# Kernel tuning notes

Hardware: AMD Instinct MI355X
Metric: run time of the kernel (lower is better)

Reference implementation:

```python
import jax, jax.numpy as jnp
import numpy as np

N_NODES = 50000
N_EDGES = 800000
F_IN = 512
HID = 256
N_CLS = 40
W_DIM = 50  # dimension*dimension*2 with dimension=5


def _prelu(x, a):
    return jnp.where(x >= 0, x, a * x)


def _segment_softmax(w, idx, n):
    # per-segment (grouped by idx), per-channel numerically stable softmax
    m = jax.ops.segment_max(w, idx, num_segments=n)
    e = jnp.exp(w - m[idx])
    s = jax.ops.segment_sum(e, idx, num_segments=n)
    return e / s[idx]


def _curvgn(x, edge_index, w_mul, W, b, w0, a, w1, b1):
    n = x.shape[0]
    h = x @ W + b                                   # [N, C]
    ow = _prelu(w_mul @ w0, a) @ w1 + b1            # [E, C] edge-weight MLP
    ow = _segment_softmax(ow, edge_index[0], n)     # softmax grouped by source (as in source)
    msg = ow * h[edge_index[0]]                     # gather x_j, weight
    return jax.ops.segment_sum(msg, edge_index[1], num_segments=n)  # scatter-add at target


def setup_inputs() -> dict:
    key = jax.random.key(0)
    ks = jax.random.split(key, 12)
    s = 0.05
    return {
        "x": jax.random.normal(ks[0], (N_NODES, F_IN), jnp.float32),
        "edge_index": jax.random.randint(ks[1], (2, N_EDGES), 0, N_NODES, jnp.int64 if jax.config.jax_enable_x64 else jnp.int32).astype(jnp.int32),
        "w_mul": jax.random.normal(ks[2], (N_EDGES, W_DIM), jnp.float32),
        "W1": jax.random.normal(ks[3], (F_IN, HID), jnp.float32) * s,
        "b1": jnp.zeros((HID,), jnp.float32),
        "m1_w0": jax.random.normal(ks[4], (W_DIM, HID), jnp.float32) * s,
        "m1_a": jnp.full((HID,), 0.2, jnp.float32),
        "m1_w1": jax.random.normal(ks[5], (HID, HID), jnp.float32) * s,
        "m1_b1": jnp.zeros((HID,), jnp.float32),
        "W2": jax.random.normal(ks[6], (HID, N_CLS), jnp.float32) * s,
        "b2": jnp.zeros((N_CLS,), jnp.float32),
        "m2_w0": jax.random.normal(ks[7], (W_DIM, N_CLS), jnp.float32) * s,
        "m2_a": jnp.full((N_CLS,), 0.2, jnp.float32),
        "m2_w1": jax.random.normal(ks[8], (N_CLS, N_CLS), jnp.float32) * s,
        "m2_b1": jnp.zeros((N_CLS,), jnp.float32),
    }


def reference(x, edge_index, w_mul, W1, b1, m1_w0, m1_a, m1_w1, m1_b1,
              W2, b2, m2_w0, m2_a, m2_w1, m2_b1):
    # eval mode: dropout is identity
    h = _curvgn(x, edge_index, w_mul, W1, b1, m1_w0, m1_a, m1_w1, m1_b1)
    h = jax.nn.elu(h)
    out = _curvgn(h, edge_index, w_mul, W2, b2, m2_w0, m2_a, m2_w1, m2_b1)
    return jax.nn.log_softmax(out, axis=1)
```

## Files before the change

kernel.cpp:

```cpp
#include <hip/hip_runtime.h>
#include <hip/hip_bf16.h>
#include <math.h>

#define N_NODESC 50000
#define N_EDGESC 800000
#define F_INC 512
#define HIDC 256
#define N_CLSC 40
#define W_DIMC 50
#define HN (2*N_NODESC)
#define NB_SCAN 196

typedef __bf16 bf16;
typedef __bf16 bf16x8 __attribute__((ext_vector_type(8)));
typedef __bf16 bf16x4 __attribute__((ext_vector_type(4)));
typedef float  f32x4  __attribute__((ext_vector_type(4)));

__global__ void k_hist(const int* __restrict__ ei, int* __restrict__ hist) {
    int e = blockIdx.x*256 + threadIdx.x;
    if (e < N_EDGESC) {
        atomicAdd(&hist[ei[e]], 1);
        atomicAdd(&hist[N_NODESC + ei[N_EDGESC + e]], 1);
    }
}
__global__ void k_copy(int* d, const int* s, int n) {
    int i = blockIdx.x*256 + threadIdx.x;
    if (i < n) d[i] = s[i];
}
__global__ void k_scan_part(const int* __restrict__ hist, int* __restrict__ part) {
    __shared__ int lds[512];
    int t = threadIdx.x;
    int i = blockIdx.x*512 + t;
    lds[t] = (i < HN) ? hist[i] : 0;
    __syncthreads();
    for (int off = 256; off > 0; off >>= 1) {
        if (t < off) lds[t] += lds[t+off];
        __syncthreads();
    }
    if (t == 0) part[blockIdx.x] = lds[0];
}
__global__ void k_scan_mid(const int* __restrict__ part, int* __restrict__ partx) {
    __shared__ int lds[256];
    int t = threadIdx.x;
    int v = (t < NB_SCAN) ? part[t] : 0;
    lds[t] = v;
    __syncthreads();
    for (int off = 1; off < 256; off <<= 1) {
        int add = (t >= off) ? lds[t-off] : 0;
        __syncthreads();
        lds[t] += add;
        __syncthreads();
    }
    partx[t] = lds[t] - v;
}
__global__ void k_scan_apply(const int* __restrict__ hist, const int* __restrict__ partx,
                             int* __restrict__ basev) {
    __shared__ int lds[512];
    int t = threadIdx.x;
    int i = blockIdx.x*512 + t;
    int v = (i < HN) ? hist[i] : 0;
    lds[t] = v;
    __syncthreads();
    for (int off = 1; off < 512; off <<= 1) {
        int add = (t >= off) ? lds[t-off] : 0;
        __syncthreads();
        lds[t] += add;
        __syncthreads();
    }
    if (i < HN) basev[i] = lds[t] - v + partx[blockIdx.x];
}
__global__ void k_scatter(const int* __restrict__ ei, int* __restrict__ cursor,
                          int* __restrict__ perm_src,
                          int* __restrict__ spd, int* __restrict__ svd) {
    int e = blockIdx.x*256 + threadIdx.x;
    if (e >= N_EDGESC) return;
    int s = ei[e];
    int d = ei[N_EDGESC + e];
    int p = atomicAdd(&cursor[s], 1);
    perm_src[p] = e;
    int q = atomicAdd(&cursor[N_NODESC + d], 1) - N_EDGESC;
    spd[q] = p;
    svd[q] = s;
}

__global__ void k_tconv(const float* __restrict__ src, bf16* __restrict__ dst,
                        int Ks, int Ns, int Kp, int Np) {
    int idx = blockIdx.x*256 + threadIdx.x;
    if (idx >= Kp*Np) return;
    int n = idx / Kp, k = idx - n*Kp;
    float v = (k < Ks && n < Ns) ? src[k*Ns + n] : 0.f;
    dst[idx] = (bf16)v;
}

__global__ __launch_bounds__(256) void k_h1(const float* __restrict__ x,
                                            const bf16* __restrict__ W1t,
                                            const float* __restrict__ b1,
                                            bf16* __restrict__ h1) {
    __shared__ __align__(16) bf16 a_lds[64*40];
    int tid = threadIdx.x;
    int lane = tid & 63, wv = tid >> 6;
    int l15 = lane & 15, quad = lane >> 4;
    int r0 = blockIdx.x * 64;
    f32x4 acc[4][4] = {};
    for (int ks = 0; ks < 16; ++ks) {
        #pragma unroll
        for (int i = 0; i < 2; ++i) {
            int idx = tid + i*256;
            int rl = idx >> 3, c4 = idx & 7;
            int rg = r0 + rl;
            f32x4 v = {};
            if (rg < N_NODESC) v = *(const f32x4*)&x[(size_t)rg*F_INC + ks*32 + c4*4];
            bf16x4 b; b[0]=(bf16)v[0]; b[1]=(bf16)v[1]; b[2]=(bf16)v[2]; b[3]=(bf16)v[3];
            *(bf16x4*)&a_lds[rl*40 + c4*4] = b;
        }
        __syncthreads();
        bf16x8 af[4], bfr[4];
        #pragma unroll
        for (int mt = 0; mt < 4; ++mt)
            af[mt] = *(const bf16x8*)&a_lds[(mt*16 + l15)*40 + quad*8];
        #pragma unroll
        for (int nt = 0; nt < 4; ++nt) {
            int n = wv*64 + nt*16 + l15;
            bfr[nt] = *(const bf16x8*)&W1t[n*F_INC + ks*32 + quad*8];
        }
        #pragma unroll
        for (int mt = 0; mt < 4; ++mt)
            #pragma unroll
            for (int nt = 0; nt < 4; ++nt)
                acc[mt][nt] = __builtin_amdgcn_mfma_f32_16x16x32_bf16(af[mt], bfr[nt], acc[mt][nt], 0, 0, 0);
        __syncthreads();
    }
    #pragma unroll
    for (int nt = 0; nt < 4; ++nt) {
        int col = wv*64 + nt*16 + l15;
        float bias = b1[col];
        #pragma unroll
        for (int mt = 0; mt < 4; ++mt)
            #pragma unroll
            for (int r = 0; r < 4; ++r) {
                int row = r0 + mt*16 + quad*4 + r;
                if (row < N_NODESC) h1[(size_t)row*HIDC + col] = (bf16)(acc[mt][nt][r] + bias);
            }
    }
}

__global__ __launch_bounds__(256) void k_edge(
    const float* __restrict__ w_mul, const int* __restrict__ perm_src,
    const int* __restrict__ ei,
    const bf16* __restrict__ w0t,  const float* __restrict__ a1,
    const bf16* __restrict__ w1t,  const float* __restrict__ bb1,
    const bf16* __restrict__ w20t, const float* __restrict__ a2,
    const bf16* __restrict__ w21t, const float* __restrict__ bb2,
    float* __restrict__ s1, float* __restrict__ s2,
    bf16* __restrict__ eow1, bf16* __restrict__ eow2) {
    __shared__ __align__(16) bf16 wm[64*72];
    __shared__ __align__(16) bf16 t1[64*264];
    __shared__ __align__(16) bf16 t2[64*72];
    __shared__ int e_lds[64], sv[64];
    int tid = threadIdx.x;
    int lane = tid & 63, wv = tid >> 6;
    int l15 = lane & 15, quad = lane >> 4;
    int p0 = blockIdx.x * 64;

    if (tid < 64) {
        int e = perm_src[p0 + tid];
        e_lds[tid] = e;
        sv[tid] = ei[e];
    }
    __syncthreads();
    #pragma unroll
    for (int i = 0; i < 16; ++i) {
        int idx = tid + i*256;
        int r = idx >> 6, k = idx & 63;
        float v = (k < W_DIMC) ? w_mul[(size_t)e_lds[r]*W_DIMC + k] : 0.f;
        wm[r*72 + k] = (bf16)v;
    }
    #pragma unroll
    for (int i = 0; i < 4; ++i) {
        int idx = tid + i*256;
        int r = idx >> 4, c = 48 + (idx & 15);
        t2[r*72 + c] = (bf16)0.f;
    }
    __syncthreads();

    {
        f32x4 acc[4][4] = {};
        #pragma unroll
        for (int ks = 0; ks < 2; ++ks) {
            bf16x8 af[4], bfr[4];
            #pragma unroll
            for (int mt = 0; mt < 4; ++mt)
                af[mt] = *(const bf16x8*)&wm[(mt*16 + l15)*72 + ks*32 + quad*8];
            #pragma unroll
            for (int i = 0; i < 4; ++i) {
                int n = wv*64 + i*16 + l15;
                bfr[i] = *(const bf16x8*)&w0t[n*64 + ks*32 + quad*8];
            }
            #pragma unroll
            for (int mt = 0; mt < 4; ++mt)
                #pragma unroll
                for (int i = 0; i < 4; ++i)
                    acc[mt][i] = __builtin_amdgcn_mfma_f32_16x16x32_bf16(af[mt], bfr[i], acc[mt][i], 0, 0, 0);
        }
        #pragma unroll
        for (int i = 0; i < 4; ++i) {
            int col = wv*64 + i*16 + l15;
            float al = a1[col];
            #pragma unroll
            for (int mt = 0; mt < 4; ++mt)
                #pragma unroll
                for (int r = 0; r < 4; ++r) {
                    float v = acc[mt][i][r];
                    v = (v >= 0.f) ? v : al*v;
                    t1[(mt*16 + quad*4 + r)*264 + col] = (bf16)v;
                }
        }
    }
    __syncthreads();

    {
        f32x4 acc[4][4] = {};
        #pragma unroll
        for (int ks = 0; ks < 8; ++ks) {
            bf16x8 af[4], bfr[4];
            #pragma unroll
            for (int mt = 0; mt < 4; ++mt)
                af[mt] = *(const bf16x8*)&t1[(mt*16 + l15)*264 + ks*32 + quad*8];
            #pragma unroll
            for (int i = 0; i < 4; ++i) {
                int n = wv*64 + i*16 + l15;
                bfr[i] = *(const bf16x8*)&w1t[n*HIDC + ks*32 + quad*8];
            }
            #pragma unroll
            for (int mt = 0; mt < 4; ++mt)
                #pragma unroll
                for (int i = 0; i < 4; ++i)
                    acc[mt][i] = __builtin_amdgcn_mfma_f32_16x16x32_bf16(af[mt], bfr[i], acc[mt][i], 0, 0, 0);
        }
        __syncthreads();
        #pragma unroll
        for (int i = 0; i < 4; ++i) {
            int col = wv*64 + i*16 + l15;
            float bias = bb1[col];
            #pragma unroll
            for (int mt = 0; mt < 4; ++mt)
                #pragma unroll
                for (int r = 0; r < 4; ++r)
                    t1[(mt*16 + quad*4 + r)*264 + col] = (bf16)__expf(acc[mt][i][r] + bias);
        }
    }
    __syncthreads();

    #pragma unroll
    for (int i = 0; i < 8; ++i) {
        int idx = i*256 + tid;
        int row = idx >> 5, c8 = idx & 31;
        bf16x8 v = *(const bf16x8*)&t1[row*264 + c8*8];
        *(bf16x8*)&eow1[(size_t)(p0 + row)*HIDC + c8*8] = v;
    }
    {
        int c = tid;
        float acc = 0.f;
        #pragma unroll 8
        for (int r = 0; r < 64; ++r) {
            acc += (float)t1[r*264 + c];
            if (r == 63 || sv[r+1] != sv[r]) {
                atomicAdd(&s1[(size_t)sv[r]*HIDC + c], acc);
                acc = 0.f;
            }
        }
    }

    {
        f32x4 acc[3] = {};
        #pragma unroll
        for (int ks = 0; ks < 2; ++ks) {
            bf16x8 af = *(const bf16x8*)&wm[(wv*16 + l15)*72 + ks*32 + quad*8];
            #pragma unroll
            for (int i = 0; i < 3; ++i) {
                bf16x8 bfr = *(const bf16x8*)&w20t[(i*16 + l15)*64 + ks*32 + quad*8];
                acc[i] = __builtin_amdgcn_mfma_f32_16x16x32_bf16(af, bfr, acc[i], 0, 0, 0);
            }
        }
        #pragma unroll
        for (int i = 0; i < 3; ++i) {
            int col = i*16 + l15;
            float al = (col < N_CLSC) ? a2[col] : 0.f;
            #pragma unroll
            for (int r = 0; r < 4; ++r) {
                float v = acc[i][r];
                v = (v >= 0.f) ? v : al*v;
                t2[(wv*16 + quad*4 + r)*72 + col] = (bf16)v;
            }
        }
    }
    __syncthreads();

    {
        f32x4 acc[3] = {};
        #pragma unroll
        for (int ks = 0; ks < 2; ++ks) {
            bf16x8 af = *(const bf16x8*)&t2[(wv*16 + l15)*72 + ks*32 + quad*8];
            #pragma unroll
            for (int i = 0; i < 3; ++i) {
                bf16x8 bfr = *(const bf16x8*)&w21t[(i*16 + l15)*64 + ks*32 + quad*8];
                acc[i] = __builtin_amdgcn_mfma_f32_16x16x32_bf16(af, bfr, acc[i], 0, 0, 0);
            }
        }
        __syncthreads();
        #pragma unroll
        for (int i = 0; i < 3; ++i) {
            int col = i*16 + l15;
            if (col < N_CLSC) {
                float bias = bb2[col];
                #pragma unroll
                for (int r = 0; r < 4; ++r)
                    t2[(wv*16 + quad*4 + r)*72 + col] = (bf16)__expf(acc[i][r] + bias);
            }
        }
    }
    __syncthreads();

    #pragma unroll
    for (int i = 0; i < 2; ++i) {
        int idx = i*256 + tid;
        if (idx < 320) {
            int row = idx / 5, c8 = idx % 5;
            bf16x8 v = *(const bf16x8*)&t2[row*72 + c8*8];
            *(bf16x8*)&eow2[(size_t)(p0 + row)*N_CLSC + c8*8] = v;
        }
    }
    if (tid < 240) {
        int c = tid % 40, g = tid / 40;
        int rA = g*11, rB = (rA + 11 < 64) ? rA + 11 : 64;
        float acc = 0.f;
        for (int r = rA; r < rB; ++r) {
            acc += (float)t2[r*72 + c];
            if (r == rB-1 || sv[r+1] != sv[r]) {
                atomicAdd(&s2[(size_t)sv[r]*N_CLSC + c], acc);
                acc = 0.f;
            }
        }
    }
}

__global__ __launch_bounds__(256) void k_agg1(
    const bf16* __restrict__ eow1, const bf16* __restrict__ g1,
    const int* __restrict__ basev, const int* __restrict__ spd,
    const int* __restrict__ svd, float* __restrict__ out1) {
    int v = blockIdx.x, c = threadIdx.x;
    int b = basev[N_NODESC + v] - N_EDGESC;
    int e = (v < N_NODESC-1) ? basev[N_NODESC + v + 1] - N_EDGESC : N_EDGESC;
    float acc = 0.f;
    #pragma unroll 2
    for (int j = b; j < e; ++j) {
        int sp = spd[j], s = svd[j];
        acc += (float)eow1[(size_t)sp*HIDC + c] * (float)g1[(size_t)s*HIDC + c];
    }
    out1[(size_t)v*HIDC + c] = (acc > 0.f) ? acc : expm1f(acc);
}

__global__ __launch_bounds__(64) void k_agg2(
    const bf16* __restrict__ eow2, const bf16* __restrict__ g2,
    const int* __restrict__ basev, const int* __restrict__ spd,
    const int* __restrict__ svd, float* __restrict__ out) {
    int v = blockIdx.x, c = threadIdx.x;
    int b = basev[N_NODESC + v] - N_EDGESC;
    int e = (v < N_NODESC-1) ? basev[N_NODESC + v + 1] - N_EDGESC : N_EDGESC;
    bool act = (c < N_CLSC);
    float acc = 0.f;
    #pragma unroll 2
    for (int j = b; j < e; ++j) {
        int sp = spd[j], s = svd[j];
        if (act) acc += (float)eow2[(size_t)sp*N_CLSC + c] * (float)g2[(size_t)s*N_CLSC + c];
    }
    float m = act ? acc : -INFINITY;
    #pragma unroll
    for (int off = 32; off > 0; off >>= 1) m = fmaxf(m, __shfl_xor(m, off));
    float ex = act ? __expf(acc - m) : 0.f;
    #pragma unroll
    for (int off = 32; off > 0; off >>= 1) ex += __shfl_xor(ex, off);
    if (act) out[(size_t)v*N_CLSC + c] = acc - m - logf(ex);
}

__global__ void k_div_bf4(bf16* __restrict__ h, const float* __restrict__ s, int n4) {
    int i = blockIdx.x*256 + threadIdx.x;
    if (i < n4) {
        bf16x4 hv = *(bf16x4*)&h[i*4];
        f32x4 sv = *(const f32x4*)&s[i*4];
        #pragma unroll
        for (int k = 0; k < 4; ++k) hv[k] = (bf16)((float)hv[k] / sv[k]);
        *(bf16x4*)&h[i*4] = hv;
    }
}
__global__ void k_h2(const float* __restrict__ out1, const float* __restrict__ W2,
                     const float* __restrict__ b2, bf16* __restrict__ h2) {
    int i = blockIdx.x*256 + threadIdx.x;
    if (i >= N_NODESC*N_CLSC) return;
    int v = i / N_CLSC, c = i - v*N_CLSC;
    float acc = b2[c];
    const float* row = &out1[(size_t)v*HIDC];
    #pragma unroll 4
    for (int k = 0; k < HIDC; ++k) acc += row[k] * W2[k*N_CLSC + c];
    h2[i] = (bf16)acc;
}

extern "C" void kernel_launch(void* const* d_in, const int* in_sizes, int n_in,
                              void* d_out, int out_size, void* d_ws, size_t ws_size,
                              hipStream_t stream) {
    const float* x    = (const float*)d_in[0];
    const int*   ei   = (const int*)d_in[1];
    const float* wmul = (const float*)d_in[2];
    const float* W1   = (const float*)d_in[3];
    const float* b1   = (const float*)d_in[4];
    const float* m1w0 = (const float*)d_in[5];
    const float* m1a  = (const float*)d_in[6];
    const float* m1w1 = (const float*)d_in[7];
    const float* m1b1 = (const float*)d_in[8];
    const float* W2   = (const float*)d_in[9];
    const float* b2   = (const float*)d_in[10];
    const float* m2w0 = (const float*)d_in[11];
    const float* m2a  = (const float*)d_in[12];
    const float* m2w1 = (const float*)d_in[13];
    const float* m2b1 = (const float*)d_in[14];
    float* out = (float*)d_out;

    char* ws = (char*)d_ws;
    size_t off = 0;
    auto alloc = [&](size_t bytes) -> void* {
        off = (off + 255) & ~(size_t)255;
        void* p = ws + off;
        off += bytes;
        return p;
    };
    bf16*  h1g1  = (bf16*) alloc((size_t)N_NODESC*HIDC*2);
    float* s1o1  = (float*)alloc((size_t)N_NODESC*HIDC*4);
    bf16*  h2g2  = (bf16*) alloc((size_t)N_NODESC*N_CLSC*2);
    float* s2    = (float*)alloc((size_t)N_NODESC*N_CLSC*4);
    bf16*  W1t   = (bf16*) alloc(256*512*2);
    bf16*  w0t   = (bf16*) alloc(256*64*2);
    bf16*  w1tm  = (bf16*) alloc(256*256*2);
    bf16*  w20t  = (bf16*) alloc(48*64*2);
    bf16*  w21t  = (bf16*) alloc(48*64*2);
    int*   hist  = (int*)  alloc(HN*4);
    int*   basev = (int*)  alloc(HN*4);
    int*   cursor= (int*)  alloc(HN*4);
    int*   part  = (int*)  alloc(256*4);
    int*   partx = (int*)  alloc(256*4);
    int*   perm_src = (int*)alloc((size_t)N_EDGESC*4);
    int*   spd      = (int*)alloc((size_t)N_EDGESC*4);
    int*   svd      = (int*)alloc((size_t)N_EDGESC*4);
    bf16*  eow1  = (bf16*) alloc((size_t)N_EDGESC*HIDC*2);
    bf16*  eow2  = (bf16*) alloc((size_t)N_EDGESC*N_CLSC*2);

    hipMemsetAsync(hist, 0, HN*4, stream);
    hipMemsetAsync(s1o1, 0, (size_t)N_NODESC*HIDC*4, stream);
    hipMemsetAsync(s2,   0, (size_t)N_NODESC*N_CLSC*4, stream);
    k_hist<<<(N_EDGESC+255)/256, 256, 0, stream>>>(ei, hist);
    k_scan_part<<<NB_SCAN, 512, 0, stream>>>(hist, part);
    k_scan_mid<<<1, 256, 0, stream>>>(part, partx);
    k_scan_apply<<<NB_SCAN, 512, 0, stream>>>(hist, partx, basev);
    k_copy<<<(HN+255)/256, 256, 0, stream>>>(cursor, basev, HN);
    k_scatter<<<(N_EDGESC+255)/256, 256, 0, stream>>>(ei, cursor, perm_src, spd, svd);

    k_tconv<<<(512*256+255)/256, 256, 0, stream>>>(W1,   W1t, 512, 256, 512, 256);
    k_tconv<<<(256*64+255)/256,  256, 0, stream>>>(m1w0, w0t,  50, 256,  64, 256);
    k_tconv<<<(256*256+255)/256, 256, 0, stream>>>(m1w1, w1tm, 256, 256, 256, 256);
    k_tconv<<<(48*64+255)/256,   256, 0, stream>>>(m2w0, w20t,  50,  40,  64,  48);
    k_tconv<<<(48*64+255)/256,   256, 0, stream>>>(m2w1, w21t,  40,  40,  64,  48);

    k_h1<<<(N_NODESC+63)/64, 256, 0, stream>>>(x, W1t, b1, h1g1);
    k_edge<<<N_EDGESC/64, 256, 0, stream>>>(wmul, perm_src, ei,
                                            w0t, m1a, w1tm, m1b1,
                                            w20t, m2a, w21t, m2b1,
                                            s1o1, s2, eow1, eow2);
    k_div_bf4<<<(N_NODESC*HIDC/4+255)/256, 256, 0, stream>>>(h1g1, s1o1, N_NODESC*HIDC/4);
    k_agg1<<<N_NODESC, 256, 0, stream>>>(eow1, h1g1, basev, spd, svd, s1o1);

    k_h2<<<(N_NODESC*N_CLSC+255)/256, 256, 0, stream>>>(s1o1, W2, b2, h2g2);
    k_div_bf4<<<(N_NODESC*N_CLSC/4+255)/256, 256, 0, stream>>>(h2g2, s2, N_NODESC*N_CLSC/4);
    k_agg2<<<N_NODESC, 64, 0, stream>>>(eow2, h2g2, basev, spd, svd, out);
}
```

Before: 1.583 ms.

## Split fused edge MLP kernel into three smaller kernels via global intermediate

Breaks the monolithic edge kernel into k_mlp1a (first layer plus PReLU, written to eow1 as a bf16 intermediate), k_mlp1b (second layer, exp, and segment-sum atomics), and k_mlp2 (the class-dimension MLP). Each kernel uses less LDS and fewer registers, which should raise occupancy and latency hiding. The w_mul gather is also vectorized to float2 loads, and w0t is staged in LDS. The cost is an extra round trip of an E x 256 bf16 tensor through global memory, w_mul being read twice, and two more launches.

```diff
diff --git a/kernel.cpp b/kernel.cpp
--- a/kernel.cpp
+++ b/kernel.cpp
@@ -14,7 +14,9 @@
 typedef __bf16 bf16;
 typedef __bf16 bf16x8 __attribute__((ext_vector_type(8)));
 typedef __bf16 bf16x4 __attribute__((ext_vector_type(4)));
+typedef __bf16 bf16x2 __attribute__((ext_vector_type(2)));
 typedef float  f32x4  __attribute__((ext_vector_type(4)));
+typedef float  f32x2  __attribute__((ext_vector_type(2)));
 
 __global__ void k_hist(const int* __restrict__ ei, int* __restrict__ hist) {
     int e = blockIdx.x*256 + threadIdx.x;
@@ -144,17 +146,155 @@
     }
 }
 
-__global__ __launch_bounds__(256) void k_edge(
+__global__ __launch_bounds__(256) void k_mlp1a(
+    const float* __restrict__ w_mul, const int* __restrict__ perm_src,
+    const bf16* __restrict__ w0t, const float* __restrict__ a1,
+    bf16* __restrict__ u1) {
+    __shared__ __align__(16) bf16 wm[64*72];
+    __shared__ __align__(16) bf16 bw[256*72];
+    __shared__ int e_lds[64];
+    int tid = threadIdx.x;
+    int lane = tid & 63, wv = tid >> 6;
+    int l15 = lane & 15, quad = lane >> 4;
+    int p0 = blockIdx.x * 64;
+
+    if (tid < 64) e_lds[tid] = perm_src[p0 + tid];
+    #pragma unroll
+    for (int i = 0; i < 8; ++i) {
+        int idx = i*256 + tid;
+        int n = idx >> 3, j = idx & 7;
+        *(bf16x8*)&bw[n*72 + j*8] = *(const bf16x8*)&w0t[n*64 + j*8];
+    }
+    __syncthreads();
+    #pragma unroll
+    for (int i = 0; i < 7; ++i) {
+        int idx = i*256 + tid;
+        if (idx < 1600) {
+            int row = idx / 25;
+            int k = 2*(idx - row*25);
+            f32x2 v = *(const f32x2*)&w_mul[(size_t)e_lds[row]*W_DIMC + k];
+            bf16x2 b; b[0] = (bf16)v[0]; b[1] = (bf16)v[1];
+            *(bf16x2*)&wm[row*72 + k] = b;
+        }
+    }
+    #pragma unroll
+    for (int i = 0; i < 2; ++i) {
+        int idx = i*256 + tid;
+        if (idx < 448) {
+            int row = idx / 7, c = 50 + 2*(idx - row*7);
+            bf16x2 z; z[0] = (bf16)0.f; z[1] = (bf16)0.f;
+            *(bf16x2*)&wm[row*72 + c] = z;
+        }
+    }
+    __syncthreads();
+
+    f32x4 acc[4][4] = {};
+    #pragma unroll
+    for (int ks = 0; ks < 2; ++ks) {
+        bf16x8 af[4], bfr[4];
+        #pragma unroll
+        for (int mt = 0; mt < 4; ++mt)
+            af[mt] = *(const bf16x8*)&wm[(mt*16 + l15)*72 + ks*32 + quad*8];
+        #pragma unroll
+        for (int i = 0; i < 4; ++i)
+            bfr[i] = *(const bf16x8*)&bw[(wv*64 + i*16 + l15)*72 + ks*32 + quad*8];
+        #pragma unroll
+        for (int mt = 0; mt < 4; ++mt)
+            #pragma unroll
+            for (int i = 0; i < 4; ++i)
+                acc[mt][i] = __builtin_amdgcn_mfma_f32_16x16x32_bf16(af[mt], bfr[i], acc[mt][i], 0, 0, 0);
+    }
+    #pragma unroll
+    for (int i = 0; i < 4; ++i) {
+        int col = wv*64 + i*16 + l15;
+        float al = a1[col];
+        #pragma unroll
+        for (int mt = 0; mt < 4; ++mt)
+            #pragma unroll
+            for (int r = 0; r < 4; ++r) {
+                float v = acc[mt][i][r];
+                v = (v >= 0.f) ? v : al*v;
+                u1[(size_t)(p0 + mt*16 + quad*4 + r)*HIDC + col] = (bf16)v;
+            }
+    }
+}
+
+__global__ __launch_bounds__(256) void k_mlp1b(
+    const int* __restrict__ perm_src, const int* __restrict__ ei,
+    const bf16* __restrict__ w1t, const float* __restrict__ bb1,
+    bf16* __restrict__ eow1,
+    float* __restrict__ s1) {
+    __shared__ __align__(16) bf16 t1[64*264];
+    __shared__ int sv[64];
+    int tid = threadIdx.x;
+    int lane = tid & 63, wv = tid >> 6;
+    int l15 = lane & 15, quad = lane >> 4;
+    int p0 = blockIdx.x * 64;
+
+    if (tid < 64) sv[tid] = ei[perm_src[p0 + tid]];
+    #pragma unroll
+    for (int i = 0; i < 8; ++i) {
+        int idx = i*256 + tid;
+        int row = idx >> 5, j = idx & 31;
+        *(bf16x8*)&t1[row*264 + j*8] = *(const bf16x8*)&eow1[(size_t)(p0 + row)*HIDC + j*8];
+    }
+    __syncthreads();
+
+    f32x4 acc[4][4] = {};
+    #pragma unroll
+    for (int ks = 0; ks < 8; ++ks) {
+        bf16x8 af[4], bfr[4];
+        #pragma unroll
+        for (int mt = 0; mt < 4; ++mt)
+            af[mt] = *(const bf16x8*)&t1[(mt*16 + l15)*264 + ks*32 + quad*8];
+        #pragma unroll
+        for (int i = 0; i < 4; ++i)
+            bfr[i] = *(const bf16x8*)&w1t[(wv*64 + i*16 + l15)*HIDC + ks*32 + quad*8];
+        #pragma unroll
+        for (int mt = 0; mt < 4; ++mt)
+            #pragma unroll
+            for (int i = 0; i < 4; ++i)
+                acc[mt][i] = __builtin_amdgcn_mfma_f32_16x16x32_bf16(af[mt], bfr[i], acc[mt][i], 0, 0, 0);
+    }
+    __syncthreads();
+    #pragma unroll
+    for (int i = 0; i < 4; ++i) {
+        int col = wv*64 + i*16 + l15;
+        float bias = bb1[col];
+        #pragma unroll
+        for (int mt = 0; mt < 4; ++mt)
+            #pragma unroll
+            for (int r = 0; r < 4; ++r)
+                t1[(mt*16 + quad*4 + r)*264 + col] = (bf16)__expf(acc[mt][i][r] + bias);
+    }
+    __syncthreads();
+    #pragma unroll
+    for (int i = 0; i < 8; ++i) {
+        int idx = i*256 + tid;
+        int row = idx >> 5, j = idx & 31;
+        *(bf16x8*)&eow1[(size_t)(p0 + row)*HIDC + j*8] = *(const bf16x8*)&t1[row*264 + j*8];
+    }
+    {
+        int c = tid;
+        float acc2 = 0.f;
+        #pragma unroll
+        for (int r = 0; r < 64; ++r) {
+            acc2 += (float)t1[r*264 + c];
+            if (r == 63 || sv[r+1] != sv[r]) {
+                atomicAdd(&s1[(size_t)sv[r]*HIDC + c], acc2);
+                acc2 = 0.f;
+            }
+        }
+    }
+}
+
+__global__ __launch_bounds__(256) void k_mlp2(
     const float* __restrict__ w_mul, const int* __restrict__ perm_src,
     const int* __restrict__ ei,
-    const bf16* __restrict__ w0t,  const float* __restrict__ a1,
-    const bf16* __restrict__ w1t,  const float* __restrict__ bb1,
     const bf16* __restrict__ w20t, const float* __restrict__ a2,
     const bf16* __restrict__ w21t, const float* __restrict__ bb2,
-    float* __restrict__ s1, float* __restrict__ s2,
-    bf16* __restrict__ eow1, bf16* __restrict__ eow2) {
+    bf16* __restrict__ eow2, float* __restrict__ s2) {
     __shared__ __align__(16) bf16 wm[64*72];
-    __shared__ __align__(16) bf16 t1[64*264];
     __shared__ __align__(16) bf16 t2[64*72];
     __shared__ int e_lds[64], sv[64];
     int tid = threadIdx.x;
@@ -169,107 +309,33 @@
     }
     __syncthreads();
     #pragma unroll
-    for (int i = 0; i < 16; ++i) {
-        int idx = tid + i*256;
-        int r = idx >> 6, k = idx & 63;
-        float v = (k < W_DIMC) ? w_mul[(size_t)e_lds[r]*W_DIMC + k] : 0.f;
-        wm[r*72 + k] = (bf16)v;
-    }
-    #pragma unroll
-    for (int i = 0; i < 4; ++i) {
-        int idx = tid + i*256;
-        int r = idx >> 4, c = 48 + (idx & 15);
-        t2[r*72 + c] = (bf16)0.f;
-    }
-    __syncthreads();
-
-    {
-        f32x4 acc[4][4] = {};
-        #pragma unroll
-        for (int ks = 0; ks < 2; ++ks) {
-            bf16x8 af[4], bfr[4];
-            #pragma unroll
-            for (int mt = 0; mt < 4; ++mt)
-                af[mt] = *(const bf16x8*)&wm[(mt*16 + l15)*72 + ks*32 + quad*8];
-            #pragma unroll
-            for (int i = 0; i < 4; ++i) {
-                int n = wv*64 + i*16 + l15;
-                bfr[i] = *(const bf16x8*)&w0t[n*64 + ks*32 + quad*8];
-            }
-            #pragma unroll
-            for (int mt = 0; mt < 4; ++mt)
-                #pragma unroll
-                for (int i = 0; i < 4; ++i)
-                    acc[mt][i] = __builtin_amdgcn_mfma_f32_16x16x32_bf16(af[mt], bfr[i], acc[mt][i], 0, 0, 0);
-        }
-        #pragma unroll
-        for (int i = 0; i < 4; ++i) {
-            int col = wv*64 + i*16 + l15;
-            float al = a1[col];
-            #pragma unroll
-            for (int mt = 0; mt < 4; ++mt)
-                #pragma unroll
-                for (int r = 0; r < 4; ++r) {
-                    float v = acc[mt][i][r];
-                    v = (v >= 0.f) ? v : al*v;
-                    t1[(mt*16 + quad*4 + r)*264 + col] = (bf16)v;
-                }
-        }
-    }
-    __syncthreads();
-
-    {
-        f32x4 acc[4][4] = {};
-        #pragma unroll
-        for (int ks = 0; ks < 8; ++ks) {
-            bf16x8 af[4], bfr[4];
-            #pragma unroll
-            for (int mt = 0; mt < 4; ++mt)
-                af[mt] = *(const bf16x8*)&t1[(mt*16 + l15)*264 + ks*32 + quad*8];
-            #pragma unroll
-            for (int i = 0; i < 4; ++i) {
-                int n = wv*64 + i*16 + l15;
-                bfr[i] = *(const bf16x8*)&w1t[n*HIDC + ks*32 + quad*8];
-            }
-            #pragma unroll
-            for (int mt = 0; mt < 4; ++mt)
-                #pragma unroll
-                for (int i = 0; i < 4; ++i)
-                    acc[mt][i] = __builtin_amdgcn_mfma_f32_16x16x32_bf16(af[mt], bfr[i], acc[mt][i], 0, 0, 0);
-        }
-        __syncthreads();
-        #pragma unroll
-        for (int i = 0; i < 4; ++i) {
-            int col = wv*64 + i*16 + l15;
-            float bias = bb1[col];
-            #pragma unroll
-            for (int mt = 0; mt < 4; ++mt)
-                #pragma unroll
-                for (int r = 0; r < 4; ++r)
-                    t1[(mt*16 + quad*4 + r)*264 + col] = (bf16)__expf(acc[mt][i][r] + bias);
-        }
-    }
-    __syncthreads();
-
-    #pragma unroll
-    for (int i = 0; i < 8; ++i) {
-        int idx = i*256 + tid;
-        int row = idx >> 5, c8 = idx & 31;
-        bf16x8 v = *(const bf16x8*)&t1[row*264 + c8*8];
-        *(bf16x8*)&eow1[(size_t)(p0 + row)*HIDC + c8*8] = v;
-    }
-    {
-        int c = tid;
-        float acc = 0.f;
-        #pragma unroll 8
-        for (int r = 0; r < 64; ++r) {
-            acc += (float)t1[r*264 + c];
-            if (r == 63 || sv[r+1] != sv[r]) {
-                atomicAdd(&s1[(size_t)sv[r]*HIDC + c], acc);
-                acc = 0.f;
-            }
-        }
-    }
+    for (int i = 0; i < 7; ++i) {
+        int idx = i*256 + tid;
+        if (idx < 1600) {
+            int row = idx / 25;
+            int k = 2*(idx - row*25);
+            f32x2 v = *(const f32x2*)&w_mul[(size_t)e_lds[row]*W_DIMC + k];
+            bf16x2 b; b[0] = (bf16)v[0]; b[1] = (bf16)v[1];
+            *(bf16x2*)&wm[row*72 + k] = b;
+        }
+    }
+    #pragma unroll
+    for (int i = 0; i < 2; ++i) {
+        int idx = i*256 + tid;
+        if (idx < 448) {
+            int row = idx / 7, c = 50 + 2*(idx - row*7);
+            bf16x2 z; z[0] = (bf16)0.f; z[1] = (bf16)0.f;
+            *(bf16x2*)&wm[row*72 + c] = z;
+        }
+    }
+    #pragma unroll
+    for (int i = 0; i < 2; ++i) {
+        int idx = i*256 + tid;
+        int row = idx >> 3, c = 48 + 2*(idx & 7);
+        bf16x2 z; z[0] = (bf16)0.f; z[1] = (bf16)0.f;
+        *(bf16x2*)&t2[row*72 + c] = z;
+    }
+    __syncthreads();
 
     {
         f32x4 acc[3] = {};
@@ -295,7 +361,6 @@
         }
     }
     __syncthreads();
-
     {
         f32x4 acc[3] = {};
         #pragma unroll
@@ -320,7 +385,6 @@
         }
     }
     __syncthreads();
-
     #pragma unroll
     for (int i = 0; i < 2; ++i) {
         int idx = i*256 + tid;
@@ -470,10 +534,10 @@
     k_tconv<<<(48*64+255)/256,   256, 0, stream>>>(m2w1, w21t,  40,  40,  64,  48);
 
     k_h1<<<(N_NODESC+63)/64, 256, 0, stream>>>(x, W1t, b1, h1g1);
-    k_edge<<<N_EDGESC/64, 256, 0, stream>>>(wmul, perm_src, ei,
-                                            w0t, m1a, w1tm, m1b1,
-                                            w20t, m2a, w21t, m2b1,
-                                            s1o1, s2, eow1, eow2);
+    k_mlp1a<<<N_EDGESC/64, 256, 0, stream>>>(wmul, perm_src, w0t, m1a, eow1);
+    k_mlp1b<<<N_EDGESC/64, 256, 0, stream>>>(perm_src, ei, w1tm, m1b1, eow1, s1o1);
+    k_mlp2<<<N_EDGESC/64, 256, 0, stream>>>(wmul, perm_src, ei, w20t, m2a, w21t, m2b1,
+                                            eow2, s2);
     k_div_bf4<<<(N_NODESC*HIDC/4+255)/256, 256, 0, stream>>>(h1g1, s1o1, N_NODESC*HIDC/4);
     k_agg1<<<N_NODESC, 256, 0, stream>>>(eow1, h1g1, basev, spd, svd, s1o1);
 
```

Result: slower. 1.745 ms (+10.2%).
